# Kernel optimization log

Hardware: AMD Instinct MI355X
Metric: run time of the kernel (lower is better)

Reference implementation:

```python
import jax, jax.numpy as jnp
import numpy as np

D_IN = 1024
D_OUT = 1024
SEQ = 4096


def setup_inputs() -> dict:
    key = jax.random.key(0)
    kx, kq, kk, kv = jax.random.split(key, 4)
    s = 1.0 / np.sqrt(D_IN)
    return {
        "x": jax.random.normal(kx, (SEQ, D_IN), dtype=jnp.float32),
        # torch Linear weights: shape [d_out, d_in], y = x @ W.T
        "Wq": jax.random.uniform(kq, (D_OUT, D_IN), jnp.float32, -s, s),
        "Wk": jax.random.uniform(kk, (D_OUT, D_IN), jnp.float32, -s, s),
        "Wv": jax.random.uniform(kv, (D_OUT, D_IN), jnp.float32, -s, s),
    }


def reference(x, Wq, Wk, Wv):
    # QKV projections (no bias)
    q = x @ Wq.T  # [N, d_out]
    k = x @ Wk.T
    v = x @ Wv.T
    scale = 1.0 / jnp.sqrt(jnp.asarray(k.shape[-1], x.dtype))
    att = jax.nn.softmax((q @ k.T) * scale, axis=-1)  # [N, N]
    return att @ v  # [N, d_out]
```

## Files before the change

### kernel.cpp

```cpp
#include <hip/hip_runtime.h>
#include <hip/hip_bf16.h>
#include <math.h>

typedef __attribute__((ext_vector_type(8))) short short8;
typedef __attribute__((ext_vector_type(4))) float floatx4;

static __device__ __forceinline__ unsigned short f2bf(float f) {
    union { float f; unsigned int u; } a; a.f = f;
    unsigned int u = a.u;
    return (unsigned short)((u + 0x7FFFu + ((u >> 16) & 1u)) >> 16);
}
static __device__ __forceinline__ float bf2f(unsigned short h) {
    union { unsigned int u; float f; } a; a.u = ((unsigned int)h) << 16;
    return a.f;
}

static __device__ __forceinline__ void cvt8(const float* __restrict__ src,
                                            unsigned short* __restrict__ dst, int i) {
    float4 v0 = *(const float4*)(src + i);
    float4 v1 = *(const float4*)(src + i + 4);
    ushort4 o0, o1;
    o0.x = f2bf(v0.x); o0.y = f2bf(v0.y); o0.z = f2bf(v0.z); o0.w = f2bf(v0.w);
    o1.x = f2bf(v1.x); o1.y = f2bf(v1.y); o1.z = f2bf(v1.z); o1.w = f2bf(v1.w);
    *(ushort4*)(dst + i) = o0;
    *(ushort4*)(dst + i + 4) = o1;
}

struct CV { const float* x; unsigned short* xb;
            const float* W[3]; unsigned short* Wb[3]; float* l; };
__global__ __launch_bounds__(256)
void cvt_all(CV a) {
    int b = blockIdx.x, t = threadIdx.x;
    if (b < 2048) {
        cvt8(a.x, a.xb, (b * 256 + t) * 8);
    } else if (b < 3584) {
        int z  = (b - 2048) >> 9;
        int bb = (b - 2048) & 511;
        cvt8(a.W[z], a.Wb[z], (bb * 256 + t) * 8);
    } else {
        float4 zz = {0.f, 0.f, 0.f, 0.f};
        #pragma unroll
        for (int c = 0; c < 4; c++)
            *(float4*)(a.l + t * 16 + c * 4) = zz;
    }
}

template<int BM, int BN, int BK, int TI, int TJ, int WCOLS>
__device__ __forceinline__ void gemm_core(const unsigned short* __restrict__ A,
                                          const unsigned short* __restrict__ B,
                                          int lda, int k_begin, int k_end,
                                          unsigned short* sA, unsigned short* sB,
                                          floatx4 (&acc)[TI][TJ],
                                          int bm, int bn)
{
    constexpr int CPR = BK / 8;
    constexpr int RPR = 2048 / BK;
    const int t    = threadIdx.x;
    const int wave = t >> 6;
    const int lane = t & 63;
    const int wm = (wave / WCOLS) * (TI * 16);
    const int wn = (wave % WCOLS) * (TJ * 16);

    const int srow   = t / CPR;
    const int schunk = t % CPR;
    const int gchunk = schunk ^ (srow & (CPR - 1));
    const int lm  = lane & 15;
    const int swz = lm & (CPR - 1);

    for (int k0 = k_begin; k0 < k_end; k0 += BK) {
        __syncthreads();
        #pragma unroll
        for (int r = 0; r < (BM * BK) / 2048; r++) {
            const unsigned short* gA =
                A + (size_t)(bm + srow + r * RPR) * lda + k0 + gchunk * 8;
            __builtin_amdgcn_global_load_lds(
                (const __attribute__((address_space(1))) void*)gA,
                (__attribute__((address_space(3))) void*)((char*)sA + wave * 1024 + r * 4096),
                16, 0, 0);
        }
        #pragma unroll
        for (int r = 0; r < (BN * BK) / 2048; r++) {
            const unsigned short* gB =
                B + (size_t)(bn + srow + r * RPR) * lda + k0 + gchunk * 8;
            __builtin_amdgcn_global_load_lds(
                (const __attribute__((address_space(1))) void*)gB,
                (__attribute__((address_space(3))) void*)((char*)sB + wave * 1024 + r * 4096),
                16, 0, 0);
        }
        __syncthreads();

        #pragma unroll
        for (int kk = 0; kk < BK; kk += 32) {
            const int c  = (kk >> 3) + (lane >> 4);
            const int ce = ((c ^ swz) << 3);
            short8 a_frag[TI], b_frag[TJ];
            #pragma unroll
            for (int i = 0; i < TI; i++)
                a_frag[i] = *(const short8*)&sA[(wm + i * 16 + lm) * BK + ce];
            #pragma unroll
            for (int j = 0; j < TJ; j++)
                b_frag[j] = *(const short8*)&sB[(wn + j * 16 + lm) * BK + ce];
            #pragma unroll
            for (int i = 0; i < TI; i++)
                #pragma unroll
                for (int j = 0; j < TJ; j++)
                    acc[i][j] = __builtin_amdgcn_mfma_f32_16x16x32_bf16(
                        a_frag[i], b_frag[j], acc[i][j], 0, 0, 0);
        }
    }
}


__device__ __forceinline__ void tile_store(unsigned short* sm,
                                           unsigned short (&vals)[4][4][4], int trans,
                                           unsigned short* __restrict__ C, int ldc,
                                           int rbase, int cbase)
{
    const int t = threadIdx.x, wave = t >> 6, lane = t & 63;
    const int wm = (wave >> 1) * 64, wn = (wave & 1) * 64;
    const int lm = lane & 15, rq = (lane >> 4) * 4;
    __syncthreads();
    #pragma unroll
    for (int i = 0; i < 4; i++)
        #pragma unroll
        for (int j = 0; j < 4; j++)
            #pragma unroll
            for (int r = 0; r < 4; r++) {
                int rr = trans ? (wn + j * 16 + lm) : (wm + i * 16 + rq + r);
                int cc = trans ? (wm + i * 16 + rq + r) : (wn + j * 16 + lm);
                sm[rr * 136 + cc] = vals[i][j][r];
            }
    __syncthreads();
    const int row = t >> 4, c16 = t & 15;
    #pragma unroll
    for (int p = 0; p < 8; p++) {
        int rr = p * 16 + row;
        short8 v = *(const short8*)&sm[rr * 136 + c16 * 8];
        *(short8*)&C[(size_t)(rbase + rr) * ldc + cbase + c16 * 8] = v;
    }
}

struct P3 { const unsigned short* W[3]; unsigned short* O[3]; };
__global__ __launch_bounds__(256)
void proj3(const unsigned short* __restrict__ xb, P3 a) {
    __shared__ unsigned short sm[17408];
    unsigned short* sA = sm;
    unsigned short* sB = sm + 8192;

    const int lid = blockIdx.x;
    const int xcd = lid & 7;
    const int rem = lid >> 3;
    const int row = (rem & 7) * 4 + (xcd >> 1);
    const int col = ((rem >> 3) & 3) * 2 + (xcd & 1);
    const int z   = rem >> 5;

    const unsigned short* B = a.W[z];
    unsigned short* O = a.O[z];
    const int trans = (z == 2);
    const float scale = (z == 0) ? 0.03125f : 1.0f;

    floatx4 acc[4][4];
    #pragma unroll
    for (int i = 0; i < 4; i++)
        #pragma unroll
        for (int j = 0; j < 4; j++) { floatx4 zz = {0.f,0.f,0.f,0.f}; acc[i][j] = zz; }

    const int bm = row * 128, bn = col * 128;
    gemm_core<128, 128, 64, 4, 4, 2>(xb, B, 1024, 0, 1024, sA, sB, acc, bm, bn);

    unsigned short vals[4][4][4];
    #pragma unroll
    for (int i = 0; i < 4; i++)
        #pragma unroll
        for (int j = 0; j < 4; j++)
            #pragma unroll
            for (int r = 0; r < 4; r++)
                vals[i][j][r] = f2bf(acc[i][j][r] * scale);

    tile_store(sm, vals, trans, O, trans ? 4096 : 1024,
               trans ? bn : bm, trans ? bm : bn);
}

__global__ __launch_bounds__(256)
void gemm_ps(const unsigned short* __restrict__ q, const unsigned short* __restrict__ k,
             unsigned short* __restrict__ Pm, float* __restrict__ l) {
    __shared__ unsigned short sm[17408];
    unsigned short* sA = sm;
    unsigned short* sB = sm + 8192;

    const int lid = blockIdx.x;
    const int xcd = lid & 7;
    const int i8  = lid >> 3;
    const int by  = (xcd & 1) * 16 + (i8 & 15);
    const int bx  = (xcd >> 1) * 8 + (i8 >> 4);

    floatx4 acc[4][4];
    #pragma unroll
    for (int i = 0; i < 4; i++)
        #pragma unroll
        for (int j = 0; j < 4; j++) { floatx4 zz = {0.f,0.f,0.f,0.f}; acc[i][j] = zz; }

    const int bm = by * 128, bn = bx * 128;
    gemm_core<128, 128, 64, 4, 4, 2>(q, k, 1024, 0, 1024, sA, sB, acc, bm, bn);

    const int lane = threadIdx.x & 63, wave = threadIdx.x >> 6;
    const int wm = (wave >> 1) * 64;
    const int lm = lane & 15, rq = (lane >> 4) * 4;
    unsigned short vals[4][4][4];
    #pragma unroll
    for (int i = 0; i < 4; i++) {
        #pragma unroll
        for (int r = 0; r < 4; r++) {
            int row = bm + wm + i * 16 + rq + r;
            float rs = 0.f;
            #pragma unroll
            for (int j = 0; j < 4; j++) {
                float e = __expf(acc[i][j][r]);
                rs += e;
                vals[i][j][r] = f2bf(e);
            }
            rs += __shfl_xor(rs, 1);
            rs += __shfl_xor(rs, 2);
            rs += __shfl_xor(rs, 4);
            rs += __shfl_xor(rs, 8);
            if (lm == 0) atomicAdd(l + row, rs);
        }
    }
    tile_store(sm, vals, 0, Pm, 4096, bm, bn);
}

__global__ __launch_bounds__(256)
void gemm_osplit(const unsigned short* __restrict__ Pm, const unsigned short* __restrict__ vT,
                 unsigned short* __restrict__ Opart) {
    __shared__ unsigned short sm[17408];
    unsigned short* sA = sm;
    unsigned short* sB = sm + 8192;

    const int lid = blockIdx.x;
    const int xcd = lid & 7;
    const int w   = lid >> 6;
    const int g   = (lid >> 3) & 7;
    const int s   = w * 8 + xcd;
    const int z   = s >> 5;
    const int row = s & 31;

    floatx4 acc[4][4];
    #pragma unroll
    for (int i = 0; i < 4; i++)
        #pragma unroll
        for (int j = 0; j < 4; j++) { floatx4 zz = {0.f,0.f,0.f,0.f}; acc[i][j] = zz; }

    const int bm = row * 128, bn = g * 128;
    gemm_core<128, 128, 64, 4, 4, 2>(Pm, vT, 4096, z * 1024, (z + 1) * 1024,
                                     sA, sB, acc, bm, bn);

    unsigned short vals[4][4][4];
    #pragma unroll
    for (int i = 0; i < 4; i++)
        #pragma unroll
        for (int j = 0; j < 4; j++)
            #pragma unroll
            for (int r = 0; r < 4; r++)
                vals[i][j][r] = f2bf(acc[i][j][r]);

    tile_store(sm, vals, 0, Opart + (size_t)z * (4096 * 1024), 1024, bm, bn);
}

__global__ __launch_bounds__(256)
void reduce_scale(const unsigned short* __restrict__ Op, const float* __restrict__ l,
                  float* __restrict__ out) {
    int i = (blockIdx.x * 256 + threadIdx.x) * 4;
    ushort4 a = *(const ushort4*)(Op + i);
    ushort4 b = *(const ushort4*)(Op + 4194304 + i);
    ushort4 c = *(const ushort4*)(Op + 8388608 + i);
    ushort4 d = *(const ushort4*)(Op + 12582912 + i);
    float inv = 1.0f / l[i >> 10];
    float4 o;
    o.x = (bf2f(a.x) + bf2f(b.x) + bf2f(c.x) + bf2f(d.x)) * inv;
    o.y = (bf2f(a.y) + bf2f(b.y) + bf2f(c.y) + bf2f(d.y)) * inv;
    o.z = (bf2f(a.z) + bf2f(b.z) + bf2f(c.z) + bf2f(d.z)) * inv;
    o.w = (bf2f(a.w) + bf2f(b.w) + bf2f(c.w) + bf2f(d.w)) * inv;
    *(float4*)(out + i) = o;
}

extern "C" void kernel_launch(void* const* d_in, const int* in_sizes, int n_in,
                              void* d_out, int out_size, void* d_ws, size_t ws_size,
                              hipStream_t stream) {
    const float* x  = (const float*)d_in[0];
    const float* Wq = (const float*)d_in[1];
    const float* Wk = (const float*)d_in[2];
    const float* Wv = (const float*)d_in[3];
    float* out = (float*)d_out;

    char* ws = (char*)d_ws;
    const size_t MB = 1u << 20;
    unsigned short* vTb = (unsigned short*)(ws);
    unsigned short* xb  = (unsigned short*)(ws + 8 * MB);
    unsigned short* Wqb = (unsigned short*)(ws + 16 * MB);
    unsigned short* Wkb = (unsigned short*)(ws + 18 * MB);
    unsigned short* Wvb = (unsigned short*)(ws + 20 * MB);
    unsigned short* qb  = (unsigned short*)(ws + 22 * MB);
    unsigned short* kb  = (unsigned short*)(ws + 30 * MB);
    unsigned short* P   = (unsigned short*)(ws + 40 * MB);
    float*          l   = (float*)(ws + 72 * MB);
    unsigned short* Opart = (unsigned short*)(ws + 8 * MB);

    dim3 blk(256);
    CV cv = {x, xb, {Wq, Wk, Wv}, {Wqb, Wkb, Wvb}, l};
    cvt_all<<<dim3(3585), blk, 0, stream>>>(cv);

    P3 p3 = {{Wqb, Wkb, Wvb}, {qb, kb, vTb}};
    proj3<<<dim3(768), blk, 0, stream>>>(xb, p3);

    gemm_ps<<<dim3(1024), blk, 0, stream>>>(qb, kb, P, l);

    gemm_osplit<<<dim3(1024), blk, 0, stream>>>(P, vTb, Opart);

    reduce_scale<<<(4096 * 1024) / 1024, blk, 0, stream>>>(Opart, l, out);
}
```

Measured before the change: 214.9 us.

## Rewrite GEMM core with hand-scheduled LDS reads, split K-halves and occupancy hints

Replaces the templated GEMM mainloop with a hand-tuned 128x128x64 core. It stages the K tile as two 32-wide halves with a new XOR swizzle and reads LDS through inline ds_read_b128 with immediate offsets. Partial lgkmcnt waits interleave fragment reads with MFMA groups, and s_setprio raises wave priority during the math phase. Kernels gain launch_bounds occupancy hints of 3 blocks per CU. The goal is to hide LDS latency and cut address arithmetic, at the cost of fragile hand-written waitcnt and barrier ordering and still no double buffering.

```diff
diff --git a/kernel.cpp b/kernel.cpp
--- a/kernel.cpp
+++ b/kernel.cpp
@@ -45,71 +45,92 @@
     }
 }
 
-template<int BM, int BN, int BK, int TI, int TJ, int WCOLS>
-__device__ __forceinline__ void gemm_core(const unsigned short* __restrict__ A,
-                                          const unsigned short* __restrict__ B,
-                                          int lda, int k_begin, int k_end,
-                                          unsigned short* sA, unsigned short* sB,
-                                          floatx4 (&acc)[TI][TJ],
-                                          int bm, int bn)
+#define DSR(dst, base, OFF)                                                    \
+    asm volatile("ds_read_b128 %0, %1 offset:%2"                               \
+                 : "=v"(dst) : "v"(base), "n"(OFF))
+#define LGKM(N) asm volatile("s_waitcnt lgkmcnt(" #N ")" ::: "memory")
+#define SBAR()  asm volatile("s_barrier" ::: "memory")
+#define SB0     __builtin_amdgcn_sched_barrier(0)
+
+typedef __attribute__((address_space(3))) char* lds3p;
+
+__device__ __forceinline__ void gemm128_core(
+    const unsigned short* __restrict__ A, const unsigned short* __restrict__ B,
+    int lda, int k_begin, int bm, int bn,
+    unsigned short* lds, floatx4 (&acc)[4][4])
 {
-    constexpr int CPR = BK / 8;
-    constexpr int RPR = 2048 / BK;
     const int t    = threadIdx.x;
     const int wave = t >> 6;
     const int lane = t & 63;
-    const int wm = (wave / WCOLS) * (TI * 16);
-    const int wn = (wave % WCOLS) * (TJ * 16);
-
-    const int srow   = t / CPR;
-    const int schunk = t % CPR;
-    const int gchunk = schunk ^ (srow & (CPR - 1));
-    const int lm  = lane & 15;
-    const int swz = lm & (CPR - 1);
-
-    for (int k0 = k_begin; k0 < k_end; k0 += BK) {
-        __syncthreads();
-        #pragma unroll
-        for (int r = 0; r < (BM * BK) / 2048; r++) {
-            const unsigned short* gA =
-                A + (size_t)(bm + srow + r * RPR) * lda + k0 + gchunk * 8;
-            __builtin_amdgcn_global_load_lds(
-                (const __attribute__((address_space(1))) void*)gA,
-                (__attribute__((address_space(3))) void*)((char*)sA + wave * 1024 + r * 4096),
-                16, 0, 0);
-        }
-        #pragma unroll
-        for (int r = 0; r < (BN * BK) / 2048; r++) {
-            const unsigned short* gB =
-                B + (size_t)(bn + srow + r * RPR) * lda + k0 + gchunk * 8;
-            __builtin_amdgcn_global_load_lds(
-                (const __attribute__((address_space(1))) void*)gB,
-                (__attribute__((address_space(3))) void*)((char*)sB + wave * 1024 + r * 4096),
-                16, 0, 0);
-        }
-        __syncthreads();
-
-        #pragma unroll
-        for (int kk = 0; kk < BK; kk += 32) {
-            const int c  = (kk >> 3) + (lane >> 4);
-            const int ce = ((c ^ swz) << 3);
-            short8 a_frag[TI], b_frag[TJ];
-            #pragma unroll
-            for (int i = 0; i < TI; i++)
-                a_frag[i] = *(const short8*)&sA[(wm + i * 16 + lm) * BK + ce];
-            #pragma unroll
-            for (int j = 0; j < TJ; j++)
-                b_frag[j] = *(const short8*)&sB[(wn + j * 16 + lm) * BK + ce];
-            #pragma unroll
-            for (int i = 0; i < TI; i++)
-                #pragma unroll
-                for (int j = 0; j < TJ; j++)
-                    acc[i][j] = __builtin_amdgcn_mfma_f32_16x16x32_bf16(
-                        a_frag[i], b_frag[j], acc[i][j], 0, 0, 0);
+    const int wrow = wave >> 1;
+    const int wcol = wave & 1;
+    const int lm   = lane & 15;
+    const int ce8  = (((lane >> 4) ^ ((lm >> 1) & 3)) << 3);
+
+    const int srow = t >> 2;
+    const int gch  = (t & 3) ^ ((srow >> 1) & 3);
+    const unsigned short* srcA = A + (size_t)(bm + srow) * lda + k_begin + gch * 8;
+    const unsigned short* srcB = B + (size_t)(bn + srow) * lda + k_begin + gch * 8;
+    const size_t rstep = (size_t)64 * lda;
+    char* ldsc = (char*)lds;
+    const int w1k = wave << 10;
+
+    lds3p lp3 = (lds3p)lds;
+    lds3p va = lp3 + ((wrow * 64 + lm) * 64 + (ce8 << 1));
+    lds3p vb = lp3 + (16384 + (wcol * 64 + lm) * 64 + (ce8 << 1));
+
+#define STAGE(kind, kh, tau) do {                                              \
+        const unsigned short* s_ = ((kind) ? srcB : srcA) + (tau) * 64 + (kh) * 32; \
+        unsigned lo_ = (kind) * 16384 + (kh) * 8192 + w1k;                     \
+        __builtin_amdgcn_global_load_lds(                                      \
+            (const __attribute__((address_space(1))) void*)s_,                 \
+            (__attribute__((address_space(3))) void*)(ldsc + lo_), 16, 0, 0);  \
+        __builtin_amdgcn_global_load_lds(                                      \
+            (const __attribute__((address_space(1))) void*)(s_ + rstep),       \
+            (__attribute__((address_space(3))) void*)(ldsc + lo_ + 4096), 16, 0, 0); \
+    } while (0)
+
+#define MFMA4(R, AV)                                                           \
+    do {                                                                       \
+        acc[R][0] = __builtin_amdgcn_mfma_f32_16x16x32_bf16(AV, b4[0], acc[R][0], 0, 0, 0); \
+        acc[R][1] = __builtin_amdgcn_mfma_f32_16x16x32_bf16(AV, b4[1], acc[R][1], 0, 0, 0); \
+        acc[R][2] = __builtin_amdgcn_mfma_f32_16x16x32_bf16(AV, b4[2], acc[R][2], 0, 0, 0); \
+        acc[R][3] = __builtin_amdgcn_mfma_f32_16x16x32_bf16(AV, b4[3], acc[R][3], 0, 0, 0); \
+    } while (0)
+
+    STAGE(0, 0, 0); STAGE(1, 0, 0); STAGE(0, 1, 0); STAGE(1, 1, 0);
+
+    short8 na[4], b4[4];
+    for (int tc = 0; tc < 16; ++tc) {
+        asm volatile("s_waitcnt vmcnt(0)" ::: "memory");
+        SBAR();
+        __builtin_amdgcn_s_setprio(1);
+        DSR(b4[0], vb, 0);    DSR(b4[1], vb, 1024);
+        DSR(b4[2], vb, 2048); DSR(b4[3], vb, 3072);
+        DSR(na[0], va, 0);    DSR(na[1], va, 1024);
+        DSR(na[2], va, 2048); DSR(na[3], va, 3072);
+        LGKM(3); SB0; MFMA4(0, na[0]);
+        LGKM(2); SB0; MFMA4(1, na[1]);
+        LGKM(1); SB0; MFMA4(2, na[2]);
+        LGKM(0); SB0; MFMA4(3, na[3]);
+        DSR(b4[0], vb, 8192);  DSR(b4[1], vb, 9216);
+        DSR(b4[2], vb, 10240); DSR(b4[3], vb, 11264);
+        DSR(na[0], va, 8192);  DSR(na[1], va, 9216);
+        DSR(na[2], va, 10240); DSR(na[3], va, 11264);
+        LGKM(3); SB0; MFMA4(0, na[0]);
+        LGKM(2); SB0; MFMA4(1, na[1]);
+        LGKM(1); SB0; MFMA4(2, na[2]);
+        LGKM(0); SB0; MFMA4(3, na[3]);
+        __builtin_amdgcn_s_setprio(0);
+        SBAR();
+        if (tc < 15) {
+            STAGE(0, 0, tc + 1); STAGE(1, 0, tc + 1);
+            STAGE(0, 1, tc + 1); STAGE(1, 1, tc + 1);
         }
     }
-}
-
+#undef STAGE
+#undef MFMA4
+}
 
 __device__ __forceinline__ void tile_store(unsigned short* sm,
                                            unsigned short (&vals)[4][4][4], int trans,
@@ -141,12 +162,9 @@
 }
 
 struct P3 { const unsigned short* W[3]; unsigned short* O[3]; };
-__global__ __launch_bounds__(256)
+__global__ __launch_bounds__(256, 3)
 void proj3(const unsigned short* __restrict__ xb, P3 a) {
-    __shared__ unsigned short sm[17408];
-    unsigned short* sA = sm;
-    unsigned short* sB = sm + 8192;
-
+    __shared__ __align__(16) unsigned short sm[17408];
     const int lid = blockIdx.x;
     const int xcd = lid & 7;
     const int rem = lid >> 3;
@@ -154,8 +172,6 @@
     const int col = ((rem >> 3) & 3) * 2 + (xcd & 1);
     const int z   = rem >> 5;
 
-    const unsigned short* B = a.W[z];
-    unsigned short* O = a.O[z];
     const int trans = (z == 2);
     const float scale = (z == 0) ? 0.03125f : 1.0f;
 
@@ -166,7 +182,7 @@
         for (int j = 0; j < 4; j++) { floatx4 zz = {0.f,0.f,0.f,0.f}; acc[i][j] = zz; }
 
     const int bm = row * 128, bn = col * 128;
-    gemm_core<128, 128, 64, 4, 4, 2>(xb, B, 1024, 0, 1024, sA, sB, acc, bm, bn);
+    gemm128_core(xb, a.W[z], 1024, 0, bm, bn, sm, acc);
 
     unsigned short vals[4][4][4];
     #pragma unroll
@@ -177,17 +193,14 @@
             for (int r = 0; r < 4; r++)
                 vals[i][j][r] = f2bf(acc[i][j][r] * scale);
 
-    tile_store(sm, vals, trans, O, trans ? 4096 : 1024,
+    tile_store(sm, vals, trans, a.O[z], trans ? 4096 : 1024,
                trans ? bn : bm, trans ? bm : bn);
 }
 
-__global__ __launch_bounds__(256)
+__global__ __launch_bounds__(256, 3)
 void gemm_ps(const unsigned short* __restrict__ q, const unsigned short* __restrict__ k,
              unsigned short* __restrict__ Pm, float* __restrict__ l) {
-    __shared__ unsigned short sm[17408];
-    unsigned short* sA = sm;
-    unsigned short* sB = sm + 8192;
-
+    __shared__ __align__(16) unsigned short sm[17408];
     const int lid = blockIdx.x;
     const int xcd = lid & 7;
     const int i8  = lid >> 3;
@@ -201,7 +214,7 @@
         for (int j = 0; j < 4; j++) { floatx4 zz = {0.f,0.f,0.f,0.f}; acc[i][j] = zz; }
 
     const int bm = by * 128, bn = bx * 128;
-    gemm_core<128, 128, 64, 4, 4, 2>(q, k, 1024, 0, 1024, sA, sB, acc, bm, bn);
+    gemm128_core(q, k, 1024, 0, bm, bn, sm, acc);
 
     const int lane = threadIdx.x & 63, wave = threadIdx.x >> 6;
     const int wm = (wave >> 1) * 64;
@@ -229,13 +242,10 @@
     tile_store(sm, vals, 0, Pm, 4096, bm, bn);
 }
 
-__global__ __launch_bounds__(256)
+__global__ __launch_bounds__(256, 3)
 void gemm_osplit(const unsigned short* __restrict__ Pm, const unsigned short* __restrict__ vT,
                  unsigned short* __restrict__ Opart) {
-    __shared__ unsigned short sm[17408];
-    unsigned short* sA = sm;
-    unsigned short* sB = sm + 8192;
-
+    __shared__ __align__(16) unsigned short sm[17408];
     const int lid = blockIdx.x;
     const int xcd = lid & 7;
     const int w   = lid >> 6;
@@ -251,8 +261,7 @@
         for (int j = 0; j < 4; j++) { floatx4 zz = {0.f,0.f,0.f,0.f}; acc[i][j] = zz; }
 
     const int bm = row * 128, bn = g * 128;
-    gemm_core<128, 128, 64, 4, 4, 2>(Pm, vT, 4096, z * 1024, (z + 1) * 1024,
-                                     sA, sB, acc, bm, bn);
+    gemm128_core(Pm, vT, 4096, z * 1024, bm, bn, sm, acc);
 
     unsigned short vals[4][4][4];
     #pragma unroll
@@ -316,5 +325,5 @@
 
     gemm_osplit<<<dim3(1024), blk, 0, stream>>>(P, vTb, Opart);
 
-    reduce_scale<<<(4096 * 1024) / 1024, blk, 0, stream>>>(Opart, l, out);
-}
+    reduce_scale<<<dim3(4096), blk, 0, stream>>>(Opart, l, out);
+}
```

New measurement: 205.5 us. 1.05x faster.
